# Performance work log

Hardware: AMD Instinct MI355X
Metric: run time of the kernel (lower is better)

The kernel has to match this reference:

```python
import jax, jax.numpy as jnp
import numpy as np

EPS = 1e-6

def setup_inputs() -> dict:
    key = jax.random.key(0)
    k1, k2, k3 = jax.random.split(key, 3)
    B, N, F, OUT = 16, 1024, 64, 128
    x = jax.random.normal(k1, (B, N, F), dtype=jnp.float32)
    A = jax.random.uniform(k2, (B, N, N), dtype=jnp.float32)
    kernel = jax.random.normal(k3, (3 * F, OUT), dtype=jnp.float32) * 0.05
    bias = jnp.zeros((OUT,), dtype=jnp.float32)
    return {"x": x, "A": A, "kernel": kernel, "bias": bias}


def reference(x, A, kernel, bias):
    # x: [B,N,F], A: [B,N,N]
    n = A.shape[-1]
    eye = jnp.eye(n, dtype=A.dtype)
    Az = A * (1.0 - eye)          # zero out diagonal (A -= diag(diag_part(A)))
    A_hat = Az + eye              # add self-loops
    deg = A_hat.sum(axis=2)       # [B,N]
    inv_asym = 1.0 / (EPS + deg)                 # D^{-1}
    s = 1.0 / (EPS + jnp.sqrt(deg))              # D^{-1/2}
    # Three message-passing variants; apply diagonal scalings as broadcasts
    o1 = jnp.matmul(Az, x)                                   # A x
    o2 = inv_asym[:, :, None] * jnp.matmul(A_hat, x)         # D^{-1} A_hat x
    o3 = s[:, :, None] * jnp.matmul(A_hat, s[:, :, None] * x)  # D^{-1/2} A_hat D^{-1/2} x
    out = jnp.concatenate([o1, o2, o3], axis=-1)             # [B,N,3F]
    out = jnp.matmul(out, kernel) + bias                     # [B,N,OUT]
    return jax.nn.relu(out)
```

## Files before the change

kernel.cpp:

```cpp
#include <hip/hip_runtime.h>
#include <hip/hip_bf16.h>
#include <cstdint>

#define NN    1024
#define FF    64
#define OUTF  128
#define KCAT  192
#define EPSV  1e-6f

typedef __attribute__((ext_vector_type(4))) float  f32x4;
typedef __attribute__((ext_vector_type(8))) __bf16 bf16x8;
typedef __attribute__((ext_vector_type(4))) __bf16 bf16x4;

#define MFMA16(a, b, c) __builtin_amdgcn_mfma_f32_16x16x32_bf16(a, b, c, 0, 0, 0)
#define GLOAD_LDS16(g, l)                                          \
    __builtin_amdgcn_global_load_lds(                              \
        (const __attribute__((address_space(1))) void*)(g),        \
        (__attribute__((address_space(3))) void*)(l), 16, 0, 0)

__global__ __launch_bounds__(256) void k_deg_cvt(const float* __restrict__ A,
                                                 float* __restrict__ d1,
                                                 float* __restrict__ sArr,
                                                 __bf16* __restrict__ Az) {
    int wave = threadIdx.x >> 6;
    int lane = threadIdx.x & 63;
    int row  = blockIdx.x * 4 + wave;
    int i    = row & (NN - 1);
    const f32x4* rp = (const f32x4*)(A + (size_t)row * NN);
    __bf16* op = Az + (size_t)row * NN;
    float sum = 0.f;
#pragma unroll
    for (int t = 0; t < 4; ++t) {
        f32x4 v = rp[t * 64 + lane];
        int base = (t * 64 + lane) * 4;
#pragma unroll
        for (int q = 0; q < 4; ++q)
            if (base + q == i) v[q] = 0.f;
        sum += v[0] + v[1] + v[2] + v[3];
        bf16x4 o;
#pragma unroll
        for (int q = 0; q < 4; ++q) o[q] = (__bf16)v[q];
        *(bf16x4*)(op + base) = o;
    }
#pragma unroll
    for (int off = 32; off; off >>= 1) sum += __shfl_xor(sum, off);
    if (lane == 0) {
        float deg = 1.0f + sum;
        d1[row]   = 1.0f / (EPSV + deg);
        sArr[row] = 1.0f / (EPSV + sqrtf(deg));
    }
}

__global__ __launch_bounds__(256) void k_prep(const float* __restrict__ x,
                                              const float* __restrict__ sArr,
                                              const float* __restrict__ kern,
                                              __bf16* __restrict__ xT,
                                              __bf16* __restrict__ sxT,
                                              __bf16* __restrict__ KT) {
    __shared__ float tile[64][65];
    int bid = blockIdx.x;
    int b   = bid >> 4;
    int k0  = (bid & 15) * 64;
    const float* xp = x + ((size_t)b * NN + k0) * FF;
    for (int i = threadIdx.x; i < 64 * 64; i += 256) {
        int r = i >> 6, c = i & 63;
        tile[r][c] = xp[r * FF + c];
    }
    __syncthreads();
    for (int i = threadIdx.x; i < 64 * 64; i += 256) {
        int c = i >> 6, kk = i & 63;
        float v  = tile[kk][c];
        float sv = v * sArr[b * NN + k0 + kk];
        size_t o = ((size_t)b * FF + c) * NN + k0 + kk;
        xT[o]  = (__bf16)v;
        sxT[o] = (__bf16)sv;
    }
    if (threadIdx.x < 96) {
        int idx = bid * 96 + threadIdx.x;
        int c = idx / KCAT;
        int k = idx - c * KCAT;
        KT[idx] = (__bf16)kern[k * OUTF + c];
    }
}

__global__ __launch_bounds__(256, 4) void k_main(const __bf16* __restrict__ Az,
                                                 const float* __restrict__ x,
                                                 const float* __restrict__ bias,
                                                 const float* __restrict__ d1g,
                                                 const float* __restrict__ sg,
                                                 const __bf16* __restrict__ xT,
                                                 const __bf16* __restrict__ sxT,
                                                 const __bf16* __restrict__ KT,
                                                 float* __restrict__ out) {
    __shared__ __align__(16) char smem[32768];

    const int tid  = threadIdx.x;
    const int w4   = tid >> 6;
    const int lane = tid & 63;
    const int l15  = lane & 15;
    const int hi   = lane >> 4;
    const int h8   = hi * 8;

    const int idx  = (blockIdx.x & 7) * 128 + (blockIdx.x >> 3);
    const int b    = idx >> 6;
    const int row0 = (idx & 63) * 16;

    {
        const __bf16* AzB = Az + (size_t)(b * NN + row0 + l15) * NN + h8;
#pragma unroll
        for (int c = 0; c < 8; ++c) {
            int t = c * 4 + w4;
            GLOAD_LDS16(AzB + t * 32, smem + t * 1024);
        }
    }

    const __bf16* xPb = xT  + ((size_t)(b * FF + w4 * 16 + l15)) * NN + h8;
    const __bf16* sPb = sxT + ((size_t)(b * FF + w4 * 16 + l15)) * NN + h8;
    const char* ldsA = smem + lane * 16;

    __syncthreads();

    f32x4 P = {}, Q = {};
#pragma unroll
    for (int t = 0; t < 32; ++t) {
        bf16x8 a  = *(const bf16x8*)(ldsA + t * 1024);
        bf16x8 xf = *(const bf16x8*)(xPb + t * 32);
        bf16x8 sf = *(const bf16x8*)(sPb + t * 32);
        P = MFMA16(a, xf, P);
        Q = MFMA16(a, sf, Q);
    }

    __syncthreads();

    __bf16 (*os)[216] = (__bf16(*)[216])smem;
#pragma unroll
    for (int j = 0; j < 4; ++j) {
        int rr   = hi * 4 + j;
        int grow = b * NN + row0 + rr;
        float dv = d1g[grow];
        float sv = sg[grow];
        int cc   = w4 * 16 + l15;
        float xv = x[(size_t)grow * FF + cc];
        os[rr][cc]       = (__bf16)P[j];
        os[rr][64 + cc]  = (__bf16)(dv * (P[j] + xv));
        os[rr][128 + cc] = (__bf16)(sv * (Q[j] + sv * xv));
    }
    __syncthreads();

    f32x4 e0 = {}, e1 = {};
#pragma unroll
    for (int ks = 0; ks < 6; ++ks) {
        bf16x8 of = *(const bf16x8*)&os[l15][ks * 32 + h8];
        bf16x8 k0 = *(const bf16x8*)&KT[(size_t)(w4 * 32 + l15) * KCAT + ks * 32 + h8];
        bf16x8 k1 = *(const bf16x8*)&KT[(size_t)(w4 * 32 + 16 + l15) * KCAT + ks * 32 + h8];
        e0 = MFMA16(k0, of, e0);
        e1 = MFMA16(k1, of, e1);
    }
    {
        const size_t orow = (size_t)(b * NN + row0 + l15) * OUTF;
#pragma unroll
        for (int g = 0; g < 2; ++g) {
            f32x4 ev = g ? e1 : e0;
            int col0 = w4 * 32 + g * 16 + hi * 4;
            f32x4 bv = *(const f32x4*)&bias[col0];
            f32x4 rv;
#pragma unroll
            for (int j = 0; j < 4; ++j) {
                float v = ev[j] + bv[j];
                rv[j] = v > 0.f ? v : 0.f;
            }
            *(f32x4*)&out[orow + col0] = rv;
        }
    }
}

extern "C" void kernel_launch(void* const* d_in, const int* in_sizes, int n_in,
                              void* d_out, int out_size, void* d_ws, size_t ws_size,
                              hipStream_t stream) {
    const float* x    = (const float*)d_in[0];
    const float* A    = (const float*)d_in[1];
    const float* kern = (const float*)d_in[2];
    const float* bias = (const float*)d_in[3];
    float* out = (float*)d_out;

    char* ws = (char*)d_ws;
    __bf16* Az  = (__bf16*)(ws);
    float*  d1  = (float*)(ws + 33554432);
    float*  s   = (float*)(ws + 33554432 + 65536);
    __bf16* xT  = (__bf16*)(ws + 33554432 + 131072);
    __bf16* sxT = (__bf16*)(ws + 33554432 + 131072 + 2097152);
    __bf16* KT  = (__bf16*)(ws + 33554432 + 131072 + 2 * 2097152);
    (void)ws_size; (void)in_sizes; (void)n_in; (void)out_size;

    k_deg_cvt<<<dim3(4096), dim3(256), 0, stream>>>(A, d1, s, Az);
    k_prep<<<dim3(256), dim3(256), 0, stream>>>(x, s, kern, xT, sxT, KT);
    k_main<<<dim3(1024), dim3(256), 0, stream>>>(Az, x, bias, d1, s, xT, sxT, KT, out);
}
```

Baseline: 150.7 us.

## Double-buffer A and x tiles in LDS with 32-row blocks in main kernel

Reworks the main aggregation kernel to process 32 rows per 512-thread block instead of 16 rows per 256-thread block. The adjacency, x and scaled-x operand slices now move through a two-stage LDS ring buffer using asynchronous global-to-LDS loads with explicit vmcnt waits and barriers. Previously the whole A strip was loaded up front and the x operands were read straight from global memory by every wave. The aim is to overlap loads with MFMA work and share the x operands across row groups. In exchange, the 80KB LDS footprint and larger blocks reduce how many blocks can be resident per CU.

```diff
diff --git a/kernel.cpp b/kernel.cpp
--- a/kernel.cpp
+++ b/kernel.cpp
@@ -83,7 +83,7 @@
     }
 }
 
-__global__ __launch_bounds__(256, 4) void k_main(const __bf16* __restrict__ Az,
+__global__ __launch_bounds__(512, 4) void k_main(const __bf16* __restrict__ Az,
                                                  const float* __restrict__ x,
                                                  const float* __restrict__ bias,
                                                  const float* __restrict__ d1g,
@@ -92,54 +92,73 @@
                                                  const __bf16* __restrict__ sxT,
                                                  const __bf16* __restrict__ KT,
                                                  float* __restrict__ out) {
-    __shared__ __align__(16) char smem[32768];
+    __shared__ __align__(16) char smem[81920];
 
     const int tid  = threadIdx.x;
-    const int w4   = tid >> 6;
+    const int w    = tid >> 6;
     const int lane = tid & 63;
     const int l15  = lane & 15;
     const int hi   = lane >> 4;
     const int h8   = hi * 8;
 
-    const int idx  = (blockIdx.x & 7) * 128 + (blockIdx.x >> 3);
-    const int b    = idx >> 6;
-    const int row0 = (idx & 63) * 16;
-
-    {
-        const __bf16* AzB = Az + (size_t)(b * NN + row0 + l15) * NN + h8;
-#pragma unroll
-        for (int c = 0; c < 8; ++c) {
-            int t = c * 4 + w4;
-            GLOAD_LDS16(AzB + t * 32, smem + t * 1024);
+    const int idx  = (blockIdx.x & 7) * 64 + (blockIdx.x >> 3);
+    const int b    = idx >> 5;
+    const int row0 = (idx & 31) * 32;
+
+    const __bf16* AzRow = Az  + (size_t)(b * NN + row0 + (w & 1) * 16 + l15) * NN
+                              + (w >> 1) * 32 + h8;
+    const __bf16* xRow  = xT  + (size_t)(b * FF + (w & 3) * 16 + l15) * NN
+                              + (w >> 2) * 32 + h8;
+    const __bf16* sxRow = sxT + (size_t)(b * FF + (w & 3) * 16 + l15) * NN
+                              + (w >> 2) * 32 + h8;
+
+#define STAGE(t, pb)                                                     \
+    {                                                                    \
+        char* bb = smem + (pb) * 40960;                                  \
+        const int kofs = (t) * 128;                                      \
+        GLOAD_LDS16(AzRow + kofs,      bb + w * 1024);                   \
+        GLOAD_LDS16(xRow + kofs,       bb + 8192  + w * 1024);           \
+        GLOAD_LDS16(xRow + kofs + 64,  bb + 8192  + (w + 8) * 1024);     \
+        GLOAD_LDS16(sxRow + kofs,      bb + 24576 + w * 1024);           \
+        GLOAD_LDS16(sxRow + kofs + 64, bb + 24576 + (w + 8) * 1024);     \
+    }
+
+    STAGE(0, 0)
+    STAGE(1, 1)
+
+    const int rg = w >> 2;
+    const int fg = w & 3;
+
+    f32x4 P = {}, Q = {};
+#pragma unroll
+    for (int t = 0; t < 8; ++t) {
+        if (t < 7) { asm volatile("s_waitcnt vmcnt(5)" ::: "memory"); }
+        else       { asm volatile("s_waitcnt vmcnt(0)" ::: "memory"); }
+        __builtin_amdgcn_s_barrier();
+        {
+            const char* bb = smem + (t & 1) * 40960;
+#pragma unroll
+            for (int ks = 0; ks < 4; ++ks) {
+                bf16x8 a  = *(const bf16x8*)(bb + (ks * 2 + rg) * 1024 + lane * 16);
+                bf16x8 xf = *(const bf16x8*)(bb + 8192  + (ks * 4 + fg) * 1024 + lane * 16);
+                bf16x8 sf = *(const bf16x8*)(bb + 24576 + (ks * 4 + fg) * 1024 + lane * 16);
+                P = MFMA16(a, xf, P);
+                Q = MFMA16(a, sf, Q);
+            }
         }
-    }
-
-    const __bf16* xPb = xT  + ((size_t)(b * FF + w4 * 16 + l15)) * NN + h8;
-    const __bf16* sPb = sxT + ((size_t)(b * FF + w4 * 16 + l15)) * NN + h8;
-    const char* ldsA = smem + lane * 16;
-
-    __syncthreads();
-
-    f32x4 P = {}, Q = {};
-#pragma unroll
-    for (int t = 0; t < 32; ++t) {
-        bf16x8 a  = *(const bf16x8*)(ldsA + t * 1024);
-        bf16x8 xf = *(const bf16x8*)(xPb + t * 32);
-        bf16x8 sf = *(const bf16x8*)(sPb + t * 32);
-        P = MFMA16(a, xf, P);
-        Q = MFMA16(a, sf, Q);
-    }
-
-    __syncthreads();
+        __builtin_amdgcn_s_barrier();
+        if (t < 6) STAGE(t + 2, t & 1)
+    }
+#undef STAGE
 
     __bf16 (*os)[216] = (__bf16(*)[216])smem;
 #pragma unroll
     for (int j = 0; j < 4; ++j) {
-        int rr   = hi * 4 + j;
+        int rr   = rg * 16 + hi * 4 + j;
         int grow = b * NN + row0 + rr;
         float dv = d1g[grow];
         float sv = sg[grow];
-        int cc   = w4 * 16 + l15;
+        int cc   = fg * 16 + l15;
         float xv = x[(size_t)grow * FF + cc];
         os[rr][cc]       = (__bf16)P[j];
         os[rr][64 + cc]  = (__bf16)(dv * (P[j] + xv));
@@ -147,21 +166,23 @@
     }
     __syncthreads();
 
+    const int rge = w >> 2;
+    const int cge = w & 3;
     f32x4 e0 = {}, e1 = {};
 #pragma unroll
     for (int ks = 0; ks < 6; ++ks) {
-        bf16x8 of = *(const bf16x8*)&os[l15][ks * 32 + h8];
-        bf16x8 k0 = *(const bf16x8*)&KT[(size_t)(w4 * 32 + l15) * KCAT + ks * 32 + h8];
-        bf16x8 k1 = *(const bf16x8*)&KT[(size_t)(w4 * 32 + 16 + l15) * KCAT + ks * 32 + h8];
+        bf16x8 of = *(const bf16x8*)&os[rge * 16 + l15][ks * 32 + h8];
+        bf16x8 k0 = *(const bf16x8*)&KT[(size_t)(cge * 32 + l15) * KCAT + ks * 32 + h8];
+        bf16x8 k1 = *(const bf16x8*)&KT[(size_t)(cge * 32 + 16 + l15) * KCAT + ks * 32 + h8];
         e0 = MFMA16(k0, of, e0);
         e1 = MFMA16(k1, of, e1);
     }
     {
-        const size_t orow = (size_t)(b * NN + row0 + l15) * OUTF;
+        const size_t orow = (size_t)(b * NN + row0 + rge * 16 + l15) * OUTF;
 #pragma unroll
         for (int g = 0; g < 2; ++g) {
             f32x4 ev = g ? e1 : e0;
-            int col0 = w4 * 32 + g * 16 + hi * 4;
+            int col0 = cge * 32 + g * 16 + hi * 4;
             f32x4 bv = *(const f32x4*)&bias[col0];
             f32x4 rv;
 #pragma unroll
@@ -194,5 +215,5 @@
 
     k_deg_cvt<<<dim3(4096), dim3(256), 0, stream>>>(A, d1, s, Az);
     k_prep<<<dim3(256), dim3(256), 0, stream>>>(x, s, kern, xT, sxT, KT);
-    k_main<<<dim3(1024), dim3(256), 0, stream>>>(Az, x, bias, d1, s, xT, sxT, KT, out);
-}
+    k_main<<<dim3(512), dim3(512), 0, stream>>>(Az, x, bias, d1, s, xT, sxT, KT, out);
+}
```

Measured after the change: 136.8 us. -9.3%, faster.
